# Kernel tuning notes

Hardware: AMD Instinct MI355X
Metric: run time of the kernel (lower is better)

## Reference

```python
import jax, jax.numpy as jnp
import numpy as np

VOCAB = 32000
EMBED = 32
HIDDEN = 16
SEQ = 128
BATCH = 32


def setup_inputs() -> dict:
    key = jax.random.key(0)
    ks = jax.random.split(key, 10)
    stdv = 1.0 / np.sqrt(HIDDEN)
    u = lambda k, shape: jax.random.uniform(k, shape, jnp.float32, -stdv, stdv)
    return {
        "input_batch": jax.random.randint(ks[0], (SEQ, BATCH), 0, VOCAB),
        "embedding": u(ks[1], (VOCAB, EMBED)),
        "W_ih": u(ks[2], (4 * HIDDEN, EMBED)),
        "W_hh": u(ks[3], (4 * HIDDEN, HIDDEN)),
        "b_ih": u(ks[4], (4 * HIDDEN,)),
        "b_hh": u(ks[5], (4 * HIDDEN,)),
        "W_out": u(ks[6], (VOCAB, HIDDEN)),
        "b_out": u(ks[7], (VOCAB,)),
        "h0": jax.random.normal(ks[8], (BATCH, HIDDEN), jnp.float32),
        "c0": jax.random.normal(ks[9], (BATCH, HIDDEN), jnp.float32),
    }


def reference(input_batch, embedding, W_ih, W_hh, b_ih, b_hh, W_out, b_out, h0, c0):
    # input_batch: [S, B] int; returns log-probs [S, B, V]
    def step(carry, idx):
        h, c = carry
        x = embedding[idx]  # [B, E] gather
        gates = x @ W_ih.T + b_ih + h @ W_hh.T + b_hh  # [B, 4H]
        i, f, g, o = jnp.split(gates, 4, axis=-1)
        c_new = jax.nn.sigmoid(f) * c + jax.nn.sigmoid(i) * jnp.tanh(g)
        h_new = jax.nn.sigmoid(o) * jnp.tanh(c_new)
        logits = h_new @ W_out.T + b_out  # [B, V]
        return (h_new, c_new), jax.nn.log_softmax(logits, axis=-1)

    _, predictions = jax.lax.scan(step, (h0, c0), input_batch)
    return predictions
```

## Files before the change

kernel.cpp:

```cpp
#include <hip/hip_runtime.h>
#include <hip/hip_bf16.h>

#define VOCAB  32000
#define EMBED  32
#define HIDDEN 16
#define SEQ    128
#define BATCH  32

typedef __attribute__((ext_vector_type(8))) short short8;
typedef __attribute__((ext_vector_type(4))) float float4v;

#define LOG2E 1.4426950408889634f
#define LN2   0.6931471805599453f

#define NSLICE 10
#define TPB    200
#define TPW    25

__device__ __forceinline__ float fexp2(float x) { return __builtin_amdgcn_exp2f(x); }
__device__ __forceinline__ float frcp(float x)  { return __builtin_amdgcn_rcpf(x); }
__device__ __forceinline__ float flog2(float x) { return __builtin_amdgcn_logf(x); }

__device__ __forceinline__ unsigned short f2bf(float x) {
    unsigned u = __float_as_uint(x);
    unsigned r = u + 0x7fffu + ((u >> 16) & 1u);
    return (unsigned short)(r >> 16);
}

__global__ __launch_bounds__(256) void k_prep(
    const float* __restrict__ emb,
    const float* __restrict__ W_ih,
    const float* __restrict__ b_ih,
    const float* __restrict__ b_hh,
    float* __restrict__ proj)
{
    int j  = threadIdx.x & 63;
    int vl = threadIdx.x >> 6;
    int vbase = blockIdx.x * 32 + vl * 8;

    float w[32];
    {
        const float4* wp = (const float4*)(W_ih + j * 32);
#pragma unroll
        for (int i = 0; i < 8; ++i) *((float4*)w + i) = wp[i];
    }
    float bias = b_ih[j] + b_hh[j];

#pragma unroll
    for (int r = 0; r < 8; ++r) {
        int v = vbase + r;
        float x[32];
        const float4* xp = (const float4*)(emb + v * 32);
#pragma unroll
        for (int i = 0; i < 8; ++i) *((float4*)x + i) = xp[i];
        float a0 = bias, a1 = 0.f;
#pragma unroll
        for (int i = 0; i < 16; ++i) {
            a0 += x[2*i]   * w[2*i];
            a1 += x[2*i+1] * w[2*i+1];
        }
        proj[(size_t)v * 64 + j] = a0 + a1;
    }
}

__global__ __launch_bounds__(256) void k_mid(
    const int* __restrict__ idx,
    const float* __restrict__ proj,
    const float* __restrict__ W_hh,
    const float* __restrict__ h0,
    const float* __restrict__ c0,
    unsigned short* __restrict__ h_ws,
    const float* __restrict__ W_out,
    const float* __restrict__ b_out,
    unsigned short* __restrict__ Wo16,
    unsigned short* __restrict__ bo16,
    float* __restrict__ gsum)
{
    int bx = blockIdx.x;
    if (bx < 32) {
        if (threadIdx.x >= 64) return;
        int b = bx;
        int j = threadIdx.x;

        float w[16];
        {
            const float4* wp = (const float4*)(W_hh + j * 16);
#pragma unroll
            for (int i = 0; i < 4; ++i) *((float4*)w + i) = wp[i];
        }

        int l15 = j & 15;
        float h = h0[b * HIDDEN + l15];
        float c = c0[b * HIDDEN + l15];

        int i0 = idx[j * BATCH + b];
        int i1 = idx[(j + 64) * BATCH + b];

        float xg0 = proj[(size_t)__shfl(i0, 0) * 64 + j];
        float xg1 = proj[(size_t)__shfl(i0, 1) * 64 + j];

        for (int s = 0; s < SEQ; ++s) {
            float xg = xg0;
            xg0 = xg1;
            if (s + 2 < SEQ) {
                int sn = s + 2;
                int idn = __shfl((sn < 64) ? i0 : i1, sn & 63);
                xg1 = proj[(size_t)idn * 64 + j];
            }

            float a0 = xg, a1 = 0.f;
#pragma unroll
            for (int k = 0; k < 8; ++k) {
                a0 += w[2*k]   * __shfl(h, 2*k);
                a1 += w[2*k+1] * __shfl(h, 2*k+1);
            }
            float acc = a0 + a1;

            float e1 = fexp2(-acc * LOG2E);
            float sg = frcp(1.f + e1);
            float e2 = fexp2(-2.f * acc * LOG2E);
            float th = 2.f * frcp(1.f + e2) - 1.f;
            float act = ((j >> 4) == 2) ? th : sg;

            float i_ = __shfl(act, l15);
            float f_ = __shfl(act, l15 + 16);
            float g_ = __shfl(act, l15 + 32);
            float o_ = __shfl(act, l15 + 48);

            c = f_ * c + i_ * g_;
            float e3 = fexp2(-2.f * c * LOG2E);
            float hc = 2.f * frcp(1.f + e3) - 1.f;
            h = o_ * hc;

            if (j < 16)
                h_ws[(size_t)(s * BATCH + b) * HIDDEN + j] = f2bf(h);
        }
    } else if (bx < 564) {
        int t4 = ((bx - 32) * 256 + threadIdx.x) * 4;
        const int NW = VOCAB * HIDDEN;
        if (t4 < NW) {
            float4 v = *(const float4*)(W_out + t4);
            Wo16[t4 + 0] = f2bf(v.x); Wo16[t4 + 1] = f2bf(v.y);
            Wo16[t4 + 2] = f2bf(v.z); Wo16[t4 + 3] = f2bf(v.w);
        } else if (t4 < NW + VOCAB) {
            int j = t4 - NW;
            float4 v = *(const float4*)(b_out + j);
            bo16[j + 0] = f2bf(v.x); bo16[j + 1] = f2bf(v.y);
            bo16[j + 2] = f2bf(v.z); bo16[j + 3] = f2bf(v.w);
        }
    } else {
        for (int i = threadIdx.x; i < 1024; i += 256)
            ((float4*)gsum)[i] = make_float4(0.f, 0.f, 0.f, 0.f);
    }
}

__global__ __launch_bounds__(512, 4) void k_lse(
    const unsigned short* __restrict__ Wo16,
    const unsigned short* __restrict__ bo16,
    const unsigned short* __restrict__ h_ws,
    float* __restrict__ gsum)
{
    __shared__ float sums[8][16];

    int bid  = blockIdx.x;
    int rg   = bid / NSLICE;
    int sl   = bid - rg * NSLICE;
    int r0   = rg * 16;
    int tid  = threadIdx.x;
    int wave = tid >> 6;
    int lane = tid & 63;
    int n = lane & 15;
    int q = lane >> 4;

    short8 bfrag = {0, 0, 0, 0, 0, 0, 0, 0};
    if (q < 2)
        bfrag = *(const short8*)(h_ws + (size_t)(r0 + n) * 16 + 8 * q);
    else if (q == 2)
        bfrag[0] = (short)0x3F80;

    int t0 = sl * TPB + wave * TPW;

    float s0 = 0.f, s1 = 0.f, s2 = 0.f, s3 = 0.f;

    for (int ss = 0; ss < 6; ++ss) {
        int tb = t0 + ss * 4;
        short8 A[4];
#pragma unroll
        for (int t = 0; t < 4; ++t) {
            short8 a = {0, 0, 0, 0, 0, 0, 0, 0};
            int v0 = (tb + t) * 16;
            if (q < 2)       a = *(const short8*)(Wo16 + (size_t)(v0 + n) * 16 + 8 * q);
            else if (q == 2) a[0] = (short)bo16[v0 + n];
            A[t] = a;
        }
#pragma unroll
        for (int t = 0; t < 4; ++t) {
            float4v dz = {0.f, 0.f, 0.f, 0.f};
            float4v d = __builtin_amdgcn_mfma_f32_16x16x32_bf16(A[t], bfrag, dz, 0, 0, 0);
            s0 += fexp2(d[0] * LOG2E);
            s1 += fexp2(d[1] * LOG2E);
            s2 += fexp2(d[2] * LOG2E);
            s3 += fexp2(d[3] * LOG2E);
        }
    }
    {
        int v0 = (t0 + 24) * 16;
        short8 a = {0, 0, 0, 0, 0, 0, 0, 0};
        if (q < 2)       a = *(const short8*)(Wo16 + (size_t)(v0 + n) * 16 + 8 * q);
        else if (q == 2) a[0] = (short)bo16[v0 + n];
        float4v dz = {0.f, 0.f, 0.f, 0.f};
        float4v d = __builtin_amdgcn_mfma_f32_16x16x32_bf16(a, bfrag, dz, 0, 0, 0);
        s0 += fexp2(d[0] * LOG2E);
        s1 += fexp2(d[1] * LOG2E);
        s2 += fexp2(d[2] * LOG2E);
        s3 += fexp2(d[3] * LOG2E);
    }

    float ssum = (s0 + s1) + (s2 + s3);
    ssum += __shfl_xor(ssum, 16);
    ssum += __shfl_xor(ssum, 32);
    if (q == 0) sums[wave][n] = ssum;
    __syncthreads();

    if (tid < 16) {
        float tot = 0.f;
#pragma unroll
        for (int wv = 0; wv < 8; ++wv) tot += sums[wv][tid];
        atomicAdd(&gsum[r0 + tid], tot);
    }
}

__global__ __launch_bounds__(512, 4) void k_write(
    const unsigned short* __restrict__ Wo16,
    const unsigned short* __restrict__ bo16,
    const unsigned short* __restrict__ h_ws,
    const float* __restrict__ gsum,
    float* __restrict__ out)
{
    __shared__ float lds[8][1024];

    int bid  = blockIdx.x;
    int rg   = bid / NSLICE;
    int sl   = bid - rg * NSLICE;
    int r0   = rg * 16;
    int tid  = threadIdx.x;
    int wave = tid >> 6;
    int lane = tid & 63;
    int n = lane & 15;
    int q = lane >> 4;
    float* wl = lds[wave];

    short8 bfrag = {0, 0, 0, 0, 0, 0, 0, 0};
    if (q < 2)
        bfrag = *(const short8*)(h_ws + (size_t)(r0 + n) * 16 + 8 * q);
    else if (q == 2)
        bfrag[0] = (short)0x3F80;

    float K = flog2(gsum[r0 + n]) * LN2;

    int t0 = sl * TPB + wave * TPW;

    for (int ss = 0; ss < 6; ++ss) {
        int tb = t0 + ss * 4;
        short8 A[4];
#pragma unroll
        for (int t = 0; t < 4; ++t) {
            short8 a = {0, 0, 0, 0, 0, 0, 0, 0};
            int v0 = (tb + t) * 16;
            if (q < 2)       a = *(const short8*)(Wo16 + (size_t)(v0 + n) * 16 + 8 * q);
            else if (q == 2) a[0] = (short)bo16[v0 + n];
            A[t] = a;
        }
#pragma unroll
        for (int t = 0; t < 4; ++t) {
            float4v dz = {0.f, 0.f, 0.f, 0.f};
            float4v d = __builtin_amdgcn_mfma_f32_16x16x32_bf16(A[t], bfrag, dz, 0, 0, 0);
            float4v ov;
            ov[0] = d[0] - K; ov[1] = d[1] - K;
            ov[2] = d[2] - K; ov[3] = d[3] - K;
            int u = t * 4 + q;
            *(float4v*)(wl + (size_t)(n * 16 + (u ^ n)) * 4) = ov;
        }
        int V0 = tb * 16;
#pragma unroll
        for (int k = 0; k < 4; ++k) {
            int rr = 4 * k + q;
            float4v val = *(const float4v*)(wl + (size_t)(rr * 16 + (n ^ rr)) * 4);
            *(float4v*)(out + (size_t)(r0 + rr) * VOCAB + V0 + n * 4) = val;
        }
    }
    {
        int v0 = (t0 + 24) * 16;
        short8 a = {0, 0, 0, 0, 0, 0, 0, 0};
        if (q < 2)       a = *(const short8*)(Wo16 + (size_t)(v0 + n) * 16 + 8 * q);
        else if (q == 2) a[0] = (short)bo16[v0 + n];
        float4v dz = {0.f, 0.f, 0.f, 0.f};
        float4v d = __builtin_amdgcn_mfma_f32_16x16x32_bf16(a, bfrag, dz, 0, 0, 0);
        float4v ov;
        ov[0] = d[0] - K; ov[1] = d[1] - K;
        ov[2] = d[2] - K; ov[3] = d[3] - K;
        *(float4v*)(out + (size_t)(r0 + n) * VOCAB + v0 + 4 * q) = ov;
    }
}

extern "C" void kernel_launch(void* const* d_in, const int* in_sizes, int n_in,
                              void* d_out, int out_size, void* d_ws, size_t ws_size,
                              hipStream_t stream)
{
    const int*   idx   = (const int*)d_in[0];
    const float* emb   = (const float*)d_in[1];
    const float* W_ih  = (const float*)d_in[2];
    const float* W_hh  = (const float*)d_in[3];
    const float* b_ih  = (const float*)d_in[4];
    const float* b_hh  = (const float*)d_in[5];
    const float* W_out = (const float*)d_in[6];
    const float* b_out = (const float*)d_in[7];
    const float* h0    = (const float*)d_in[8];
    const float* c0    = (const float*)d_in[9];

    char* p = (char*)d_ws;
    float*          proj = (float*)p;                      p += (size_t)VOCAB * 64 * 4;
    unsigned short* Wo16 = (unsigned short*)p;             p += (size_t)VOCAB * 16 * 2;
    unsigned short* bo16 = (unsigned short*)p;             p += (size_t)VOCAB * 2;
    unsigned short* h_ws = (unsigned short*)p;             p += (size_t)SEQ * BATCH * HIDDEN * 2;
    float*          gsum = (float*)p;

    k_prep<<<1000, 256, 0, stream>>>(emb, W_ih, b_ih, b_hh, proj);
    k_mid<<<565, 256, 0, stream>>>(idx, proj, W_hh, h0, c0, h_ws,
                                   W_out, b_out, Wo16, bo16, gsum);
    k_lse<<<SEQ * BATCH / 16 * NSLICE, 512, 0, stream>>>(Wo16, bo16, h_ws, gsum);
    k_write<<<SEQ * BATCH / 16 * NSLICE, 512, 0, stream>>>(Wo16, bo16, h_ws, gsum,
                                                           (float*)d_out);
}
```

Baseline: 698.7 us.

## Fuse embedding input projection into recurrent kernel and use nontemporal output stores

Removes the precomputation kernel that projected the whole 32000-row embedding table through W_ih. The recurrent kernel instead gathers only the needed embedding rows, double-buffered two steps ahead, and computes the input gates inline. This saves one launch and about 8 MB of writes plus the later reads, in exchange for more per-step arithmetic and registers on the serial LSTM path. Output stores in the write kernel become nontemporal to avoid polluting caches with the large log-prob tensor.

```diff
diff --git a/kernel.cpp b/kernel.cpp
--- a/kernel.cpp
+++ b/kernel.cpp
@@ -27,46 +27,13 @@
     return (unsigned short)(r >> 16);
 }
 
-__global__ __launch_bounds__(256) void k_prep(
+__global__ __launch_bounds__(256) void k_mid(
+    const int* __restrict__ idx,
     const float* __restrict__ emb,
     const float* __restrict__ W_ih,
+    const float* __restrict__ W_hh,
     const float* __restrict__ b_ih,
     const float* __restrict__ b_hh,
-    float* __restrict__ proj)
-{
-    int j  = threadIdx.x & 63;
-    int vl = threadIdx.x >> 6;
-    int vbase = blockIdx.x * 32 + vl * 8;
-
-    float w[32];
-    {
-        const float4* wp = (const float4*)(W_ih + j * 32);
-#pragma unroll
-        for (int i = 0; i < 8; ++i) *((float4*)w + i) = wp[i];
-    }
-    float bias = b_ih[j] + b_hh[j];
-
-#pragma unroll
-    for (int r = 0; r < 8; ++r) {
-        int v = vbase + r;
-        float x[32];
-        const float4* xp = (const float4*)(emb + v * 32);
-#pragma unroll
-        for (int i = 0; i < 8; ++i) *((float4*)x + i) = xp[i];
-        float a0 = bias, a1 = 0.f;
-#pragma unroll
-        for (int i = 0; i < 16; ++i) {
-            a0 += x[2*i]   * w[2*i];
-            a1 += x[2*i+1] * w[2*i+1];
-        }
-        proj[(size_t)v * 64 + j] = a0 + a1;
-    }
-}
-
-__global__ __launch_bounds__(256) void k_mid(
-    const int* __restrict__ idx,
-    const float* __restrict__ proj,
-    const float* __restrict__ W_hh,
     const float* __restrict__ h0,
     const float* __restrict__ c0,
     unsigned short* __restrict__ h_ws,
@@ -82,12 +49,19 @@
         int b = bx;
         int j = threadIdx.x;
 
-        float w[16];
+        float wih[32];
+        {
+            const float4* wp = (const float4*)(W_ih + j * 32);
+#pragma unroll
+            for (int i = 0; i < 8; ++i) *((float4*)wih + i) = wp[i];
+        }
+        float whh[16];
         {
             const float4* wp = (const float4*)(W_hh + j * 16);
 #pragma unroll
-            for (int i = 0; i < 4; ++i) *((float4*)w + i) = wp[i];
-        }
+            for (int i = 0; i < 4; ++i) *((float4*)whh + i) = wp[i];
+        }
+        float bias = b_ih[j] + b_hh[j];
 
         int l15 = j & 15;
         float h = h0[b * HIDDEN + l15];
@@ -96,45 +70,68 @@
         int i0 = idx[j * BATCH + b];
         int i1 = idx[(j + 64) * BATCH + b];
 
-        float xg0 = proj[(size_t)__shfl(i0, 0) * 64 + j];
-        float xg1 = proj[(size_t)__shfl(i0, 1) * 64 + j];
-
-        for (int s = 0; s < SEQ; ++s) {
-            float xg = xg0;
-            xg0 = xg1;
-            if (s + 2 < SEQ) {
-                int sn = s + 2;
-                int idn = __shfl((sn < 64) ? i0 : i1, sn & 63);
-                xg1 = proj[(size_t)idn * 64 + j];
-            }
-
-            float a0 = xg, a1 = 0.f;
-#pragma unroll
-            for (int k = 0; k < 8; ++k) {
-                a0 += w[2*k]   * __shfl(h, 2*k);
-                a1 += w[2*k+1] * __shfl(h, 2*k+1);
-            }
-            float acc = a0 + a1;
-
-            float e1 = fexp2(-acc * LOG2E);
-            float sg = frcp(1.f + e1);
-            float e2 = fexp2(-2.f * acc * LOG2E);
-            float th = 2.f * frcp(1.f + e2) - 1.f;
-            float act = ((j >> 4) == 2) ? th : sg;
-
-            float i_ = __shfl(act, l15);
-            float f_ = __shfl(act, l15 + 16);
-            float g_ = __shfl(act, l15 + 32);
-            float o_ = __shfl(act, l15 + 48);
-
-            c = f_ * c + i_ * g_;
-            float e3 = fexp2(-2.f * c * LOG2E);
-            float hc = 2.f * frcp(1.f + e3) - 1.f;
-            h = o_ * hc;
-
-            if (j < 16)
-                h_ws[(size_t)(s * BATCH + b) * HIDDEN + j] = f2bf(h);
-        }
+        float XA[32], XB[32];
+        {
+            int v0 = __builtin_amdgcn_readfirstlane(__shfl(i0, 0));
+            const float4* ep = (const float4*)(emb + (size_t)v0 * 32);
+#pragma unroll
+            for (int i = 0; i < 8; ++i) *((float4*)XA + i) = ep[i];
+            int v1 = __builtin_amdgcn_readfirstlane(__shfl(i0, 1));
+            const float4* eq = (const float4*)(emb + (size_t)v1 * 32);
+#pragma unroll
+            for (int i = 0; i < 8; ++i) *((float4*)XB + i) = eq[i];
+        }
+
+#define LSTM_STEP(XBUF, s)                                                    \
+        {                                                                     \
+               \
+            float g0 = 0.f, g1 = 0.f, g2 = 0.f, g3 = 0.f;                     \
+            _Pragma("unroll")                                                 \
+            for (int i = 0; i < 8; ++i) {                                     \
+                g0 += XBUF[4*i]   * wih[4*i];                                 \
+                g1 += XBUF[4*i+1] * wih[4*i+1];                               \
+                g2 += XBUF[4*i+2] * wih[4*i+2];                               \
+                g3 += XBUF[4*i+3] * wih[4*i+3];                               \
+            }                                                                 \
+            float xg = bias + ((g0 + g1) + (g2 + g3));                        \
+                          \
+            if ((s) + 2 < SEQ) {                                              \
+                int sn = (s) + 2;                                             \
+                int vn = __shfl((sn < 64) ? i0 : i1, sn & 63);                \
+                int vs = __builtin_amdgcn_readfirstlane(vn);                  \
+                const float4* ep = (const float4*)(emb + (size_t)vs * 32);    \
+                _Pragma("unroll")                                             \
+                for (int i = 0; i < 8; ++i) *((float4*)XBUF + i) = ep[i];     \
+            }                                                                 \
+            float a0 = 0.f, a1 = 0.f;                                         \
+            _Pragma("unroll")                                                 \
+            for (int k = 0; k < 8; ++k) {                                     \
+                a0 += whh[2*k]   * __shfl(h, 2*k);                            \
+                a1 += whh[2*k+1] * __shfl(h, 2*k+1);                          \
+            }                                                                 \
+            float acc = xg + a0 + a1;                                         \
+            float e1 = fexp2(-acc * LOG2E);                                   \
+            float sg = frcp(1.f + e1);                                        \
+            float e2 = fexp2(-2.f * acc * LOG2E);                             \
+            float th = 2.f * frcp(1.f + e2) - 1.f;                            \
+            float act = ((j >> 4) == 2) ? th : sg;                            \
+            float i_ = __shfl(act, l15);                                      \
+            float f_ = __shfl(act, l15 + 16);                                 \
+            float g_ = __shfl(act, l15 + 32);                                 \
+            float o_ = __shfl(act, l15 + 48);                                 \
+            c = f_ * c + i_ * g_;                                             \
+            float e3 = fexp2(-2.f * c * LOG2E);                               \
+            float hc = 2.f * frcp(1.f + e3) - 1.f;                            \
+            h = o_ * hc;                                                      \
+            if (j < 16)                                                       \
+                h_ws[(size_t)((s) * BATCH + b) * HIDDEN + j] = f2bf(h);       \
+        }
+
+        for (int s = 0; s < SEQ; s += 2) {
+            LSTM_STEP(XA, s)
+            LSTM_STEP(XB, s + 1)
+        }
+#undef LSTM_STEP
     } else if (bx < 564) {
         int t4 = ((bx - 32) * 256 + threadIdx.x) * 4;
         const int NW = VOCAB * HIDDEN;
@@ -286,7 +283,8 @@
         for (int k = 0; k < 4; ++k) {
             int rr = 4 * k + q;
             float4v val = *(const float4v*)(wl + (size_t)(rr * 16 + (n ^ rr)) * 4);
-            *(float4v*)(out + (size_t)(r0 + rr) * VOCAB + V0 + n * 4) = val;
+            __builtin_nontemporal_store(val,
+                (float4v*)(out + (size_t)(r0 + rr) * VOCAB + V0 + n * 4));
         }
     }
     {
@@ -299,7 +297,8 @@
         float4v ov;
         ov[0] = d[0] - K; ov[1] = d[1] - K;
         ov[2] = d[2] - K; ov[3] = d[3] - K;
-        *(float4v*)(out + (size_t)(r0 + n) * VOCAB + v0 + 4 * q) = ov;
+        __builtin_nontemporal_store(ov,
+            (float4v*)(out + (size_t)(r0 + n) * VOCAB + v0 + 4 * q));
     }
 }
 
@@ -319,15 +318,13 @@
     const float* c0    = (const float*)d_in[9];
 
     char* p = (char*)d_ws;
-    float*          proj = (float*)p;                      p += (size_t)VOCAB * 64 * 4;
     unsigned short* Wo16 = (unsigned short*)p;             p += (size_t)VOCAB * 16 * 2;
     unsigned short* bo16 = (unsigned short*)p;             p += (size_t)VOCAB * 2;
     unsigned short* h_ws = (unsigned short*)p;             p += (size_t)SEQ * BATCH * HIDDEN * 2;
     float*          gsum = (float*)p;
 
-    k_prep<<<1000, 256, 0, stream>>>(emb, W_ih, b_ih, b_hh, proj);
-    k_mid<<<565, 256, 0, stream>>>(idx, proj, W_hh, h0, c0, h_ws,
-                                   W_out, b_out, Wo16, bo16, gsum);
+    k_mid<<<565, 256, 0, stream>>>(idx, emb, W_ih, W_hh, b_ih, b_hh, h0, c0,
+                                   h_ws, W_out, b_out, Wo16, bo16, gsum);
     k_lse<<<SEQ * BATCH / 16 * NSLICE, 512, 0, stream>>>(Wo16, bo16, h_ws, gsum);
     k_write<<<SEQ * BATCH / 16 * NSLICE, 512, 0, stream>>>(Wo16, bo16, h_ws, gsum,
                                                            (float*)d_out);
```

Result: slower. 721.0 us (+3.2%).

## Fuse logsumexp and output write kernels into one per-row-group kernel

Applied to the files above, without the earlier changes.

Merges the separate sum-of-exp and write kernels into a single kernel where each 1024-thread block handles 16 rows across the whole vocabulary, reducing the softmax normaliser in shared memory instead of via global atomics. This removes the gsum buffer, its zeroing, the atomics and one kernel launch, and folds the -K subtraction into the MFMA accumulator init. The trade-off is a much smaller grid (256 blocks) with 64KB LDS per block, lowering occupancy and parallelism for the bandwidth-bound output write.

```diff
diff --git a/kernel.cpp b/kernel.cpp
--- a/kernel.cpp
+++ b/kernel.cpp
@@ -13,9 +13,7 @@
 #define LOG2E 1.4426950408889634f
 #define LN2   0.6931471805599453f
 
-#define NSLICE 10
-#define TPB    200
-#define TPW    25
+#define TPW_OUT 125
 
 __device__ __forceinline__ float fexp2(float x) { return __builtin_amdgcn_exp2f(x); }
 __device__ __forceinline__ float frcp(float x)  { return __builtin_amdgcn_rcpf(x); }
@@ -73,8 +71,7 @@
     const float* __restrict__ W_out,
     const float* __restrict__ b_out,
     unsigned short* __restrict__ Wo16,
-    unsigned short* __restrict__ bo16,
-    float* __restrict__ gsum)
+    unsigned short* __restrict__ bo16)
 {
     int bx = blockIdx.x;
     if (bx < 32) {
@@ -135,7 +132,7 @@
             if (j < 16)
                 h_ws[(size_t)(s * BATCH + b) * HIDDEN + j] = f2bf(h);
         }
-    } else if (bx < 564) {
+    } else {
         int t4 = ((bx - 32) * 256 + threadIdx.x) * 4;
         const int NW = VOCAB * HIDDEN;
         if (t4 < NW) {
@@ -148,24 +145,19 @@
             bo16[j + 0] = f2bf(v.x); bo16[j + 1] = f2bf(v.y);
             bo16[j + 2] = f2bf(v.z); bo16[j + 3] = f2bf(v.w);
         }
-    } else {
-        for (int i = threadIdx.x; i < 1024; i += 256)
-            ((float4*)gsum)[i] = make_float4(0.f, 0.f, 0.f, 0.f);
-    }
-}
-
-__global__ __launch_bounds__(512, 4) void k_lse(
+    }
+}
+
+__global__ __launch_bounds__(1024, 4) void k_out(
     const unsigned short* __restrict__ Wo16,
     const unsigned short* __restrict__ bo16,
     const unsigned short* __restrict__ h_ws,
-    float* __restrict__ gsum)
-{
-    __shared__ float sums[8][16];
-
-    int bid  = blockIdx.x;
-    int rg   = bid / NSLICE;
-    int sl   = bid - rg * NSLICE;
-    int r0   = rg * 16;
+    float* __restrict__ out)
+{
+    __shared__ float sums[16][16];
+    __shared__ float lds[16][1024];
+
+    int r0   = blockIdx.x * 16;
     int tid  = threadIdx.x;
     int wave = tid >> 6;
     int lane = tid & 63;
@@ -178,11 +170,11 @@
     else if (q == 2)
         bfrag[0] = (short)0x3F80;
 
-    int t0 = sl * TPB + wave * TPW;
+    const int t0 = wave * TPW_OUT;
 
     float s0 = 0.f, s1 = 0.f, s2 = 0.f, s3 = 0.f;
 
-    for (int ss = 0; ss < 6; ++ss) {
+    for (int ss = 0; ss < 31; ++ss) {
         int tb = t0 + ss * 4;
         short8 A[4];
 #pragma unroll
@@ -204,7 +196,7 @@
         }
     }
     {
-        int v0 = (t0 + 24) * 16;
+        int v0 = (t0 + 124) * 16;
         short8 a = {0, 0, 0, 0, 0, 0, 0, 0};
         if (q < 2)       a = *(const short8*)(Wo16 + (size_t)(v0 + n) * 16 + 8 * q);
         else if (q == 2) a[0] = (short)bo16[v0 + n];
@@ -222,45 +214,14 @@
     if (q == 0) sums[wave][n] = ssum;
     __syncthreads();
 
-    if (tid < 16) {
-        float tot = 0.f;
-#pragma unroll
-        for (int wv = 0; wv < 8; ++wv) tot += sums[wv][tid];
-        atomicAdd(&gsum[r0 + tid], tot);
-    }
-}
-
-__global__ __launch_bounds__(512, 4) void k_write(
-    const unsigned short* __restrict__ Wo16,
-    const unsigned short* __restrict__ bo16,
-    const unsigned short* __restrict__ h_ws,
-    const float* __restrict__ gsum,
-    float* __restrict__ out)
-{
-    __shared__ float lds[8][1024];
-
-    int bid  = blockIdx.x;
-    int rg   = bid / NSLICE;
-    int sl   = bid - rg * NSLICE;
-    int r0   = rg * 16;
-    int tid  = threadIdx.x;
-    int wave = tid >> 6;
-    int lane = tid & 63;
-    int n = lane & 15;
-    int q = lane >> 4;
+    float tot = 0.f;
+#pragma unroll
+    for (int wv = 0; wv < 16; ++wv) tot += sums[wv][n];
+    float K = flog2(tot) * LN2;
+    float4v cinit = {-K, -K, -K, -K};
+
     float* wl = lds[wave];
-
-    short8 bfrag = {0, 0, 0, 0, 0, 0, 0, 0};
-    if (q < 2)
-        bfrag = *(const short8*)(h_ws + (size_t)(r0 + n) * 16 + 8 * q);
-    else if (q == 2)
-        bfrag[0] = (short)0x3F80;
-
-    float K = flog2(gsum[r0 + n]) * LN2;
-
-    int t0 = sl * TPB + wave * TPW;
-
-    for (int ss = 0; ss < 6; ++ss) {
+    for (int ss = 0; ss < 31; ++ss) {
         int tb = t0 + ss * 4;
         short8 A[4];
 #pragma unroll
@@ -273,13 +234,9 @@
         }
 #pragma unroll
         for (int t = 0; t < 4; ++t) {
-            float4v dz = {0.f, 0.f, 0.f, 0.f};
-            float4v d = __builtin_amdgcn_mfma_f32_16x16x32_bf16(A[t], bfrag, dz, 0, 0, 0);
-            float4v ov;
-            ov[0] = d[0] - K; ov[1] = d[1] - K;
-            ov[2] = d[2] - K; ov[3] = d[3] - K;
+            float4v d = __builtin_amdgcn_mfma_f32_16x16x32_bf16(A[t], bfrag, cinit, 0, 0, 0);
             int u = t * 4 + q;
-            *(float4v*)(wl + (size_t)(n * 16 + (u ^ n)) * 4) = ov;
+            *(float4v*)(wl + (size_t)(n * 16 + (u ^ n)) * 4) = d;
         }
         int V0 = tb * 16;
 #pragma unroll
@@ -290,16 +247,12 @@
         }
     }
     {
-        int v0 = (t0 + 24) * 16;
+        int v0 = (t0 + 124) * 16;
         short8 a = {0, 0, 0, 0, 0, 0, 0, 0};
         if (q < 2)       a = *(const short8*)(Wo16 + (size_t)(v0 + n) * 16 + 8 * q);
         else if (q == 2) a[0] = (short)bo16[v0 + n];
-        float4v dz = {0.f, 0.f, 0.f, 0.f};
-        float4v d = __builtin_amdgcn_mfma_f32_16x16x32_bf16(a, bfrag, dz, 0, 0, 0);
-        float4v ov;
-        ov[0] = d[0] - K; ov[1] = d[1] - K;
-        ov[2] = d[2] - K; ov[3] = d[3] - K;
-        *(float4v*)(out + (size_t)(r0 + n) * VOCAB + v0 + 4 * q) = ov;
+        float4v d = __builtin_amdgcn_mfma_f32_16x16x32_bf16(a, bfrag, cinit, 0, 0, 0);
+        *(float4v*)(out + (size_t)(r0 + n) * VOCAB + v0 + 4 * q) = d;
     }
 }
 
@@ -322,13 +275,10 @@
     float*          proj = (float*)p;                      p += (size_t)VOCAB * 64 * 4;
     unsigned short* Wo16 = (unsigned short*)p;             p += (size_t)VOCAB * 16 * 2;
     unsigned short* bo16 = (unsigned short*)p;             p += (size_t)VOCAB * 2;
-    unsigned short* h_ws = (unsigned short*)p;             p += (size_t)SEQ * BATCH * HIDDEN * 2;
-    float*          gsum = (float*)p;
+    unsigned short* h_ws = (unsigned short*)p;
 
     k_prep<<<1000, 256, 0, stream>>>(emb, W_ih, b_ih, b_hh, proj);
-    k_mid<<<565, 256, 0, stream>>>(idx, proj, W_hh, h0, c0, h_ws,
-                                   W_out, b_out, Wo16, bo16, gsum);
-    k_lse<<<SEQ * BATCH / 16 * NSLICE, 512, 0, stream>>>(Wo16, bo16, h_ws, gsum);
-    k_write<<<SEQ * BATCH / 16 * NSLICE, 512, 0, stream>>>(Wo16, bo16, h_ws, gsum,
-                                                           (float*)d_out);
-}
+    k_mid<<<564, 256, 0, stream>>>(idx, proj, W_hh, h0, c0, h_ws,
+                                   W_out, b_out, Wo16, bo16);
+    k_out<<<SEQ * BATCH / 16, 1024, 0, stream>>>(Wo16, bo16, h_ws, (float*)d_out);
+}
```

New measurement: 740.3 us. +5.9%, slower.
